# Optimization experiments

Hardware: AMD Instinct MI355X
Metric: run time of the kernel (lower is better)

## Reference

```python
import jax, jax.numpy as jnp
import numpy as np

N_BINS = 10
THRESHOLD = 0.5
FOR_NEG_CLASS = False


def reference(outputs, labels):
    """Single-pass equivalent of CalibrationCurve.update starting from zeroed buffers.

    Returns jnp.stack([prob_sum, tp_sum, count]) of shape (3, N_BINS).
    Bin b covers (low[b], high[b]] with edges = linspace(-1e-6, 1, N_BINS+1),
    exactly matching the torch per-bin masked reductions, fused into one
    bucketize + three segment-sums (one HBM pass instead of 3*N_BINS).
    """
    if FOR_NEG_CLASS:
        outputs = 1.0 - outputs
        labels = 1.0 - labels
    edges = jnp.linspace(jnp.float32(-1e-6), jnp.float32(1.0), N_BINS + 1)
    high = edges[1:]   # upper bound per bin (inclusive)
    low0 = edges[0]    # global lower bound (exclusive)

    x = outputs.ravel()
    y = labels.ravel()
    # smallest b with x <= high[b]  (side='left': high[b-1] < x <= high[b])
    bin_idx = jnp.searchsorted(high, x, side='left')
    valid = (x > low0) & (x <= high[-1])
    # invalid elements get index N_BINS -> dropped by segment_sum (out of range)
    idx = jnp.where(valid, bin_idx, N_BINS)

    prob_sum = jax.ops.segment_sum(x, idx, num_segments=N_BINS)
    tp_sum = jax.ops.segment_sum((y > THRESHOLD).astype(jnp.float32), idx, num_segments=N_BINS)
    count = jax.ops.segment_sum(jnp.ones_like(x), idx, num_segments=N_BINS)
    return jnp.stack([prob_sum, tp_sum, count])  # (3, N_BINS)


def setup_inputs() -> dict:
    key = jax.random.key(0)
    k1, k2 = jax.random.split(key)
    outputs = jax.random.uniform(k1, (32, 1024, 1024), dtype=jnp.float32)
    labels = jax.random.uniform(k2, (32, 1024, 1024), dtype=jnp.float32)
    return {"outputs": outputs, "labels": labels}
```

## Files before the change

kernel.cpp:

```cpp
#include <hip/hip_runtime.h>

#define NBINS 10
#define ROWW  22
#define PART_STRIDE 32

__global__ __launch_bounds__(256) void calib_hist(
    const float* __restrict__ outputs,
    const float* __restrict__ labels,
    float* __restrict__ partials,
    long n)
{
    __shared__ __align__(16) unsigned int s_hist[256 * ROWW];

    const int tid = threadIdx.x;
    for (int j = tid; j < 256 * ROWW; j += 256) s_hist[j] = 0u;
    __syncthreads();

    const float low0 = -1e-6f;
    const float step = (1.0f - low0) / 10.0f;
    unsigned int* __restrict__ row = &s_hist[tid * ROWW];

    const long total4 = n >> 2;
    const float4* o4 = (const float4*)outputs;
    const float4* l4 = (const float4*)labels;
    const long gid = (long)blockIdx.x * blockDim.x + tid;
    const long gsz = (long)gridDim.x * blockDim.x;

    for (long i = gid; i < total4; i += gsz) {
        float4 o = o4[i];
        float4 l = l4[i];
        float xs[4] = {o.x, o.y, o.z, o.w};
        float ys[4] = {l.x, l.y, l.z, l.w};
#pragma unroll
        for (int k = 0; k < 4; ++k) {
            float x = xs[k];
            bool valid = (x > low0) & (x <= 1.0f);
            int e = (int)(x * 10.0f);
            e = e < 0 ? 0 : (e > 9 ? 9 : e);
            float fe  = (float)e;
            float hb0 = fmaf(fe,        step, low0);
            float hb1 = fmaf(fe + 1.0f, step, low0);
            int b = e + ((x > hb1) ? 1 : 0) - (((e > 0) & (x <= hb0)) ? 1 : 0);
            b = b < 0 ? 0 : (b > 9 ? 9 : b);
            float        px = valid ? x : 0.0f;
            unsigned int pc = valid ? ((ys[k] > 0.5f) ? 0x10001u : 1u) : 0u;
            unsigned long long* p = (unsigned long long*)&row[2 * b];
            unsigned long long v = *p;
            float        pr = __uint_as_float((unsigned int)v) + px;
            unsigned int ct = (unsigned int)(v >> 32) + pc;
            *p = ((unsigned long long)ct << 32) | (unsigned long long)__float_as_uint(pr);
        }
    }

    const long tail0 = total4 << 2;
    for (long j = tail0 + gid; j < n; j += gsz) {
        float x = outputs[j];
        float y = labels [j];
        bool valid = (x > low0) & (x <= 1.0f);
        int e = (int)(x * 10.0f);
        e = e < 0 ? 0 : (e > 9 ? 9 : e);
        float fe  = (float)e;
        float hb0 = fmaf(fe,        step, low0);
        float hb1 = fmaf(fe + 1.0f, step, low0);
        int b = e + ((x > hb1) ? 1 : 0) - (((e > 0) & (x <= hb0)) ? 1 : 0);
        b = b < 0 ? 0 : (b > 9 ? 9 : b);
        float        px = valid ? x : 0.0f;
        unsigned int pc = valid ? ((y > 0.5f) ? 0x10001u : 1u) : 0u;
        unsigned long long* p = (unsigned long long*)&row[2 * b];
        unsigned long long v = *p;
        float        pr = __uint_as_float((unsigned int)v) + px;
        unsigned int ct = (unsigned int)(v >> 32) + pc;
        *p = ((unsigned long long)ct << 32) | (unsigned long long)__float_as_uint(pr);
    }

    __syncthreads();

    if (tid < 240) {
        int slot  = tid % 30;
        int chunk = tid / 30;
        int b = slot % NBINS;
        float acc = 0.0f;
        int r0 = chunk * 32;
        for (int r = r0; r < r0 + 32; ++r) {
            unsigned int base = (unsigned int)r * ROWW + 2 * b;
            if (slot < NBINS) {
                acc += __uint_as_float(s_hist[base]);
            } else {
                unsigned int c = s_hist[base + 1];
                acc += (slot < 2 * NBINS) ? (float)(c >> 16) : (float)(c & 0xFFFFu);
            }
        }
        ((float*)s_hist)[(unsigned int)(chunk * 30 + slot) * ROWW + 20] = acc;
    }
    __syncthreads();
    if (tid < 3 * NBINS) {
        float s = 0.0f;
#pragma unroll
        for (int c = 0; c < 8; ++c)
            s += ((float*)s_hist)[(unsigned int)(c * 30 + tid) * ROWW + 20];
        partials[(long)blockIdx.x * PART_STRIDE + tid] = s;
    }
}

__global__ __launch_bounds__(256) void calib_reduce(
    const float* __restrict__ partials, float* __restrict__ out, int nrows)
{
    const int s   = blockIdx.x;
    const int tid = threadIdx.x;
    double acc = 0.0;
    for (int r = tid; r < nrows; r += 256)
        acc += (double)partials[(long)r * PART_STRIDE + s];
#pragma unroll
    for (int off = 32; off > 0; off >>= 1)
        acc += __shfl_down(acc, off, 64);
    __shared__ double wsum[4];
    if ((tid & 63) == 0) wsum[tid >> 6] = acc;
    __syncthreads();
    if (tid == 0) out[s] = (float)(wsum[0] + wsum[1] + wsum[2] + wsum[3]);
}

extern "C" void kernel_launch(void* const* d_in, const int* in_sizes, int n_in,
                              void* d_out, int out_size, void* d_ws, size_t ws_size,
                              hipStream_t stream) {
    const float* outputs = (const float*)d_in[0];
    const float* labels  = (const float*)d_in[1];
    float* out = (float*)d_out;
    long n = (long)in_sizes[0];

    int nblocks = 1792;
    size_t need = (size_t)nblocks * PART_STRIDE * sizeof(float);
    if (ws_size < need) {
        nblocks = (int)(ws_size / (PART_STRIDE * sizeof(float)));
        if (nblocks < 1) nblocks = 1;
    }
    float* partials = (float*)d_ws;

    calib_hist  <<<nblocks, 256, 0, stream>>>(outputs, labels, partials, n);
    calib_reduce<<<3 * NBINS, 256, 0, stream>>>(partials, out, nblocks);
}
```

Before: 279.6 us.

## Replace per-thread LDS histogram with register accumulators and prefetch next loads

Each thread now keeps its 10-bin sums and packed counts in registers, updated with predicated adds across all bins, instead of read-modify-write on a private LDS row. The block reduction becomes wave shuffles plus a small shared array, and the main loop software-prefetches the next float4 pair. Block count rises from 1792 to 2048. This drops LDS traffic and the LDS footprint, which limited occupancy, but costs about ten times more ALU work per element.

```diff
diff --git a/kernel.cpp b/kernel.cpp
--- a/kernel.cpp
+++ b/kernel.cpp
@@ -1,7 +1,6 @@
 #include <hip/hip_runtime.h>
 
 #define NBINS 10
-#define ROWW  22
 #define PART_STRIDE 32
 
 __global__ __launch_bounds__(256) void calib_hist(
@@ -10,15 +9,14 @@
     float* __restrict__ partials,
     long n)
 {
-    __shared__ __align__(16) unsigned int s_hist[256 * ROWW];
-
     const int tid = threadIdx.x;
-    for (int j = tid; j < 256 * ROWW; j += 256) s_hist[j] = 0u;
-    __syncthreads();
-
     const float low0 = -1e-6f;
     const float step = (1.0f - low0) / 10.0f;
-    unsigned int* __restrict__ row = &s_hist[tid * ROWW];
+
+    float        pacc[NBINS];
+    unsigned int cacc[NBINS];
+#pragma unroll
+    for (int j = 0; j < NBINS; ++j) { pacc[j] = 0.0f; cacc[j] = 0u; }
 
     const long total4 = n >> 2;
     const float4* o4 = (const float4*)outputs;
@@ -26,36 +24,48 @@
     const long gid = (long)blockIdx.x * blockDim.x + tid;
     const long gsz = (long)gridDim.x * blockDim.x;
 
-    for (long i = gid; i < total4; i += gsz) {
+    long i = gid;
+    if (i < total4) {
         float4 o = o4[i];
         float4 l = l4[i];
-        float xs[4] = {o.x, o.y, o.z, o.w};
-        float ys[4] = {l.x, l.y, l.z, l.w};
+        for (;;) {
+            const long nexti = i + gsz;
+            const bool have_next = (nexti < total4);
+            float4 no, nl;
+            if (have_next) { no = o4[nexti]; nl = l4[nexti]; }
+
+            float xs[4] = {o.x, o.y, o.z, o.w};
+            float ys[4] = {l.x, l.y, l.z, l.w};
 #pragma unroll
-        for (int k = 0; k < 4; ++k) {
-            float x = xs[k];
-            bool valid = (x > low0) & (x <= 1.0f);
-            int e = (int)(x * 10.0f);
-            e = e < 0 ? 0 : (e > 9 ? 9 : e);
-            float fe  = (float)e;
-            float hb0 = fmaf(fe,        step, low0);
-            float hb1 = fmaf(fe + 1.0f, step, low0);
-            int b = e + ((x > hb1) ? 1 : 0) - (((e > 0) & (x <= hb0)) ? 1 : 0);
-            b = b < 0 ? 0 : (b > 9 ? 9 : b);
-            float        px = valid ? x : 0.0f;
-            unsigned int pc = valid ? ((ys[k] > 0.5f) ? 0x10001u : 1u) : 0u;
-            unsigned long long* p = (unsigned long long*)&row[2 * b];
-            unsigned long long v = *p;
-            float        pr = __uint_as_float((unsigned int)v) + px;
-            unsigned int ct = (unsigned int)(v >> 32) + pc;
-            *p = ((unsigned long long)ct << 32) | (unsigned long long)__float_as_uint(pr);
+            for (int k = 0; k < 4; ++k) {
+                float x = xs[k];
+                bool valid = (x > low0) & (x <= 1.0f);
+                int e = (int)(x * 10.0f);
+                e = e < 0 ? 0 : (e > 9 ? 9 : e);
+                float fe  = (float)e;
+                float hb0 = fmaf(fe,        step, low0);
+                float hb1 = fmaf(fe + 1.0f, step, low0);
+                int b = e + ((x > hb1) ? 1 : 0) - (((e > 0) & (x <= hb0)) ? 1 : 0);
+                b = b < 0 ? 0 : (b > 9 ? 9 : b);
+                b = valid ? b : NBINS;
+                unsigned int pc = (ys[k] > 0.5f) ? 0x10001u : 1u;
+#pragma unroll
+                for (int j = 0; j < NBINS; ++j) {
+                    bool hit = (b == j);
+                    pacc[j] += hit ? x : 0.0f;
+                    cacc[j] += hit ? pc : 0u;
+                }
+            }
+
+            if (!have_next) break;
+            o = no; l = nl; i = nexti;
         }
     }
 
     const long tail0 = total4 << 2;
-    for (long j = tail0 + gid; j < n; j += gsz) {
-        float x = outputs[j];
-        float y = labels [j];
+    for (long t = tail0 + gid; t < n; t += gsz) {
+        float x = outputs[t];
+        float y = labels [t];
         bool valid = (x > low0) & (x <= 1.0f);
         int e = (int)(x * 10.0f);
         e = e < 0 ? 0 : (e > 9 ? 9 : e);
@@ -64,40 +74,39 @@
         float hb1 = fmaf(fe + 1.0f, step, low0);
         int b = e + ((x > hb1) ? 1 : 0) - (((e > 0) & (x <= hb0)) ? 1 : 0);
         b = b < 0 ? 0 : (b > 9 ? 9 : b);
-        float        px = valid ? x : 0.0f;
-        unsigned int pc = valid ? ((y > 0.5f) ? 0x10001u : 1u) : 0u;
-        unsigned long long* p = (unsigned long long*)&row[2 * b];
-        unsigned long long v = *p;
-        float        pr = __uint_as_float((unsigned int)v) + px;
-        unsigned int ct = (unsigned int)(v >> 32) + pc;
-        *p = ((unsigned long long)ct << 32) | (unsigned long long)__float_as_uint(pr);
+        b = valid ? b : NBINS;
+        unsigned int pc = (y > 0.5f) ? 0x10001u : 1u;
+#pragma unroll
+        for (int j = 0; j < NBINS; ++j) {
+            bool hit = (b == j);
+            pacc[j] += hit ? x : 0.0f;
+            cacc[j] += hit ? pc : 0u;
+        }
     }
 
-    __syncthreads();
-
-    if (tid < 240) {
-        int slot  = tid % 30;
-        int chunk = tid / 30;
-        int b = slot % NBINS;
-        float acc = 0.0f;
-        int r0 = chunk * 32;
-        for (int r = r0; r < r0 + 32; ++r) {
-            unsigned int base = (unsigned int)r * ROWW + 2 * b;
-            if (slot < NBINS) {
-                acc += __uint_as_float(s_hist[base]);
-            } else {
-                unsigned int c = s_hist[base + 1];
-                acc += (slot < 2 * NBINS) ? (float)(c >> 16) : (float)(c & 0xFFFFu);
-            }
+    __shared__ float s_red[4][32];
+    const int lane = tid & 63;
+    const int wave = tid >> 6;
+#pragma unroll
+    for (int j = 0; j < NBINS; ++j) {
+        float p  = pacc[j];
+        float tp = (float)(cacc[j] >> 16);
+        float ct = (float)(cacc[j] & 0xFFFFu);
+#pragma unroll
+        for (int off = 32; off > 0; off >>= 1) {
+            p  += __shfl_xor(p,  off, 64);
+            tp += __shfl_xor(tp, off, 64);
+            ct += __shfl_xor(ct, off, 64);
         }
-        ((float*)s_hist)[(unsigned int)(chunk * 30 + slot) * ROWW + 20] = acc;
+        if (lane == 0) {
+            s_red[wave][j]             = p;
+            s_red[wave][NBINS + j]     = tp;
+            s_red[wave][2 * NBINS + j] = ct;
+        }
     }
     __syncthreads();
     if (tid < 3 * NBINS) {
-        float s = 0.0f;
-#pragma unroll
-        for (int c = 0; c < 8; ++c)
-            s += ((float*)s_hist)[(unsigned int)(c * 30 + tid) * ROWW + 20];
+        float s = s_red[0][tid] + s_red[1][tid] + s_red[2][tid] + s_red[3][tid];
         partials[(long)blockIdx.x * PART_STRIDE + tid] = s;
     }
 }
@@ -127,7 +136,7 @@
     float* out = (float*)d_out;
     long n = (long)in_sizes[0];
 
-    int nblocks = 1792;
+    int nblocks = 2048;
     size_t need = (size_t)nblocks * PART_STRIDE * sizeof(float);
     if (ws_size < need) {
         nblocks = (int)(ws_size / (PART_STRIDE * sizeof(float)));
```

Result: slower. 289.2 us (+3.4%).

## Software-pipeline batched float4 loads and shrink per-thread histogram rows

Applied to the files above, without the earlier changes.

The main loop now loads four float4 pairs per thread and prefetches the next batch while the current one is binned into the per-thread LDS histogram. The goal is more memory-level parallelism on this bandwidth-bound streaming pass. The per-thread LDS row shrinks from 22 to 20 words, the final in-block reduction is rebuilt around warp-shuffles across half-wavefronts, and the grid grows from 1792 to 2048 blocks. The prefetch raises register pressure, and the 20-word row stride may change LDS bank-conflict behaviour.

```diff
diff --git a/kernel.cpp b/kernel.cpp
--- a/kernel.cpp
+++ b/kernel.cpp
@@ -1,8 +1,37 @@
 #include <hip/hip_runtime.h>
 
 #define NBINS 10
-#define ROWW  22
+#define ROWW  20
 #define PART_STRIDE 32
+#define BATCH 4
+
+__device__ __forceinline__ void process4(const float4& o, const float4& l,
+                                         unsigned int* __restrict__ row)
+{
+    const float low0 = -1e-6f;
+    const float step = (1.0f - low0) / 10.0f;
+    float xs[4] = {o.x, o.y, o.z, o.w};
+    float ys[4] = {l.x, l.y, l.z, l.w};
+#pragma unroll
+    for (int k = 0; k < 4; ++k) {
+        float x = xs[k];
+        bool valid = (x > low0) & (x <= 1.0f);
+        int e = (int)(x * 10.0f);
+        e = e < 0 ? 0 : (e > 9 ? 9 : e);
+        float fe  = (float)e;
+        float hb0 = fmaf(fe,        step, low0);
+        float hb1 = fmaf(fe + 1.0f, step, low0);
+        int b = e + ((x > hb1) ? 1 : 0) - (((e > 0) & (x <= hb0)) ? 1 : 0);
+        b = b < 0 ? 0 : (b > 9 ? 9 : b);
+        float        px = valid ? x : 0.0f;
+        unsigned int pc = valid ? ((ys[k] > 0.5f) ? 0x10001u : 1u) : 0u;
+        unsigned long long* p = (unsigned long long*)&row[2 * b];
+        unsigned long long v = *p;
+        float        pr = __uint_as_float((unsigned int)v) + px;
+        unsigned int ct = (unsigned int)(v >> 32) + pc;
+        *p = ((unsigned long long)ct << 32) | (unsigned long long)__float_as_uint(pr);
+    }
+}
 
 __global__ __launch_bounds__(256) void calib_hist(
     const float* __restrict__ outputs,
@@ -16,8 +45,6 @@
     for (int j = tid; j < 256 * ROWW; j += 256) s_hist[j] = 0u;
     __syncthreads();
 
-    const float low0 = -1e-6f;
-    const float step = (1.0f - low0) / 10.0f;
     unsigned int* __restrict__ row = &s_hist[tid * ROWW];
 
     const long total4 = n >> 2;
@@ -25,37 +52,49 @@
     const float4* l4 = (const float4*)labels;
     const long gid = (long)blockIdx.x * blockDim.x + tid;
     const long gsz = (long)gridDim.x * blockDim.x;
+    const long bstep = (long)BATCH * gsz;
 
-    for (long i = gid; i < total4; i += gsz) {
+    long i = gid;
+    if (i + (BATCH - 1) * gsz < total4) {
+        float4 co[BATCH], cl[BATCH];
+#pragma unroll
+        for (int q = 0; q < BATCH; ++q) {
+            co[q] = o4[i + q * gsz];
+            cl[q] = l4[i + q * gsz];
+        }
+        for (;;) {
+            const long ni = i + bstep;
+            const bool hn = (ni + (BATCH - 1) * gsz < total4);
+            float4 no_[BATCH], nl_[BATCH];
+            if (hn) {
+#pragma unroll
+                for (int q = 0; q < BATCH; ++q) {
+                    no_[q] = o4[ni + q * gsz];
+                    nl_[q] = l4[ni + q * gsz];
+                }
+            }
+#pragma unroll
+            for (int q = 0; q < BATCH; ++q)
+                process4(co[q], cl[q], row);
+            if (!hn) break;
+#pragma unroll
+            for (int q = 0; q < BATCH; ++q) { co[q] = no_[q]; cl[q] = nl_[q]; }
+            i = ni;
+        }
+        i += bstep;
+    }
+    for (; i < total4; i += gsz) {
         float4 o = o4[i];
         float4 l = l4[i];
-        float xs[4] = {o.x, o.y, o.z, o.w};
-        float ys[4] = {l.x, l.y, l.z, l.w};
-#pragma unroll
-        for (int k = 0; k < 4; ++k) {
-            float x = xs[k];
-            bool valid = (x > low0) & (x <= 1.0f);
-            int e = (int)(x * 10.0f);
-            e = e < 0 ? 0 : (e > 9 ? 9 : e);
-            float fe  = (float)e;
-            float hb0 = fmaf(fe,        step, low0);
-            float hb1 = fmaf(fe + 1.0f, step, low0);
-            int b = e + ((x > hb1) ? 1 : 0) - (((e > 0) & (x <= hb0)) ? 1 : 0);
-            b = b < 0 ? 0 : (b > 9 ? 9 : b);
-            float        px = valid ? x : 0.0f;
-            unsigned int pc = valid ? ((ys[k] > 0.5f) ? 0x10001u : 1u) : 0u;
-            unsigned long long* p = (unsigned long long*)&row[2 * b];
-            unsigned long long v = *p;
-            float        pr = __uint_as_float((unsigned int)v) + px;
-            unsigned int ct = (unsigned int)(v >> 32) + pc;
-            *p = ((unsigned long long)ct << 32) | (unsigned long long)__float_as_uint(pr);
-        }
+        process4(o, l, row);
     }
 
+    const float low0 = -1e-6f;
+    const float step = (1.0f - low0) / 10.0f;
     const long tail0 = total4 << 2;
-    for (long j = tail0 + gid; j < n; j += gsz) {
-        float x = outputs[j];
-        float y = labels [j];
+    for (long t = tail0 + gid; t < n; t += gsz) {
+        float x = outputs[t];
+        float y = labels [t];
         bool valid = (x > low0) & (x <= 1.0f);
         int e = (int)(x * 10.0f);
         e = e < 0 ? 0 : (e > 9 ? 9 : e);
@@ -75,12 +114,12 @@
 
     __syncthreads();
 
-    if (tid < 240) {
-        int slot  = tid % 30;
-        int chunk = tid / 30;
-        int b = slot % NBINS;
-        float acc = 0.0f;
-        int r0 = chunk * 32;
+    const int slot  = tid & 31;
+    const int group = tid >> 5;
+    float acc = 0.0f;
+    if (slot < 3 * NBINS) {
+        const int b  = slot % NBINS;
+        const int r0 = group * 32;
         for (int r = r0; r < r0 + 32; ++r) {
             unsigned int base = (unsigned int)r * ROWW + 2 * b;
             if (slot < NBINS) {
@@ -90,14 +129,15 @@
                 acc += (slot < 2 * NBINS) ? (float)(c >> 16) : (float)(c & 0xFFFFu);
             }
         }
-        ((float*)s_hist)[(unsigned int)(chunk * 30 + slot) * ROWW + 20] = acc;
     }
+    acc += __shfl_xor(acc, 32, 64);
+    __syncthreads();
+    if ((tid & 63) < 32 && slot < 3 * NBINS)
+        ((float*)s_hist)[(tid >> 6) * 32 + slot] = acc;
     __syncthreads();
     if (tid < 3 * NBINS) {
-        float s = 0.0f;
-#pragma unroll
-        for (int c = 0; c < 8; ++c)
-            s += ((float*)s_hist)[(unsigned int)(c * 30 + tid) * ROWW + 20];
+        float* sh = (float*)s_hist;
+        float s = sh[tid] + sh[32 + tid] + sh[64 + tid] + sh[96 + tid];
         partials[(long)blockIdx.x * PART_STRIDE + tid] = s;
     }
 }
@@ -127,7 +167,7 @@
     float* out = (float*)d_out;
     long n = (long)in_sizes[0];
 
-    int nblocks = 1792;
+    int nblocks = 2048;
     size_t need = (size_t)nblocks * PART_STRIDE * sizeof(float);
     if (ws_size < need) {
         nblocks = (int)(ws_size / (PART_STRIDE * sizeof(float)));
```

Result: slower. 288.5 us (+3.2%).
